# Optimization experiments

Measured on AMD Instinct MI355X. Metric: run time of the kernel, lower is better.

Reference implementation:

```python
import jax, jax.numpy as jnp
import numpy as np

# Straight-through binarization: forward hard threshold, backward identity.
# Matches BinarizeTensorThresh / BinarizedLinearFunction / BinaryActivation STE
# semantics from the diffnaps my_layers module (grad_weight = g^T x, i.e. the
# continuous weight receives the gradient of the binary weight unchanged).

def make_ste(thresh):
    @jax.custom_vjp
    def f(x):
        return (x >= thresh).astype(x.dtype)
    def fwd(x):
        return f(x), None
    def bwd(_, g):
        return (g,)
    f.defvjp(fwd, bwd)
    return f

ste_half = make_ste(0.5)  # weight binarization threshold (the 0.5 ctor arg)
ste_one = make_ste(1.0)   # activation fires when (pre-act + bias) >= 1

B, D, H, L = 4096, 5000, 2000, 50  # batch, input_dim(items), hidden_dim(patterns), label_dim
DATA_SPARSITY = 0.05


def setup_inputs() -> dict:
    key = jax.random.key(0)
    k = jax.random.split(key, 5)
    # sparse binary transaction data
    x = (jax.random.uniform(k[0], (B, D)) < DATA_SPARSITY).astype(jnp.float32)
    # continuous encoder weight in [0,1); binarized at 0.5 inside forward
    W_enc = jax.random.uniform(k[1], (H, D), dtype=jnp.float32)
    # small negative encoder bias (BinaPs-style init)
    b_enc = -jnp.abs(jax.random.normal(k[2], (H,), dtype=jnp.float32)) * 0.1
    act0_bias = jnp.zeros((H,), jnp.float32)
    act3_bias = jnp.zeros((D,), jnp.float32)
    # classifier_weight = logit(clip(N(0.1, 0.1), 0.01, 0.99)) as in __init__
    y = jnp.clip(0.1 + 0.1 * jax.random.normal(k[3], (L, H), dtype=jnp.float32), 0.01, 0.99)
    classifier_weight = jnp.log(y / (1.0 - y))
    return {
        "x": x,
        "W_enc": W_enc,
        "b_enc": b_enc,
        "act0_bias": act0_bias,
        "act3_bias": act3_bias,
        "classifier_weight": classifier_weight,
    }


def reference(x, W_enc, b_enc, act0_bias, act3_bias, classifier_weight):
    # fc0_enc: binarized-weight linear with bias
    Wb = ste_half(W_enc)                       # [H, D] in {0,1}
    h = x @ Wb.T + b_enc                       # [B, H]
    # act0: binary activation (threshold 1 on biased pre-activation)
    z = ste_one(h + act0_bias)                 # [B, H]
    # classify: sigmoid-gated classifier head (external_classifier=None / mode 'None')
    final_w = jax.nn.sigmoid(classifier_weight / 0.5)  # [L, H]
    classification = z @ final_w.T             # [B, L]
    # fc3_dec: shares the binarized encoder weight, transposed, no bias
    xd = z @ Wb                                # [B, D]
    output = ste_one(xd + act3_bias)           # [B, D]
    return output, classification, z
```

## Files before the change

### kernel.cpp

```cpp
#include <hip/hip_runtime.h>
#include <stdint.h>

static constexpr int Bn = 4096;
static constexpr int Dn = 5000;
static constexpr int Hn = 2000;
static constexpr int Ln = 50;
static constexpr int XW = 80;
static constexpr int Hpad = 2048;
static constexpr int Dpad = 5120;

typedef int v4i __attribute__((ext_vector_type(4)));
typedef int v16i __attribute__((ext_vector_type(16)));

#if defined(__has_builtin)
#if __has_builtin(__builtin_amdgcn_global_load_lds)
#define HAVE_GLOAD_LDS 1
#endif
#endif

#ifdef HAVE_GLOAD_LDS
__device__ __forceinline__ void gload16(const uint8_t* g, uint8_t* l) {
  __builtin_amdgcn_global_load_lds(
      (const __attribute__((address_space(1))) uint32_t*)g,
      (__attribute__((address_space(3))) uint32_t*)l, 16, 0, 0);
}
#endif

__device__ __forceinline__ int popc_acc(uint64_t v, int acc) {
  acc = __builtin_popcount((uint32_t)v) + acc;
  acc = __builtin_popcount((uint32_t)(v >> 32)) + acc;
  return acc;
}

__global__ void k_pack_xT(const float* __restrict__ x, uint8_t* __restrict__ xiT) {
  int g = (int)blockIdx.x * 256 + (int)threadIdx.x;
  int kb = g >> 12;
  int row = g & 4095;
  if (kb >= Dpad / 16) return;
  uint8_t o[16];
  int c0 = kb * 16;
  if (c0 + 15 < Dn) {
#pragma unroll
    for (int q = 0; q < 4; ++q) {
      float4 v = *(const float4*)(x + (size_t)row * Dn + c0 + q * 4);
      o[q * 4 + 0] = v.x >= 0.5f;
      o[q * 4 + 1] = v.y >= 0.5f;
      o[q * 4 + 2] = v.z >= 0.5f;
      o[q * 4 + 3] = v.w >= 0.5f;
    }
  } else {
#pragma unroll
    for (int e = 0; e < 16; ++e) {
      int c = c0 + e;
      o[e] = (c < Dn) ? (x[(size_t)row * Dn + c] >= 0.5f ? 1 : 0) : 0;
    }
  }
  *(uint4*)(xiT + ((size_t)kb * Bn + row) * 16) = *(uint4*)o;
}

__global__ __launch_bounds__(256) void k_pack_w_dualT(const float* __restrict__ W,
                                                      uint8_t* __restrict__ wi8T,
                                                      uint8_t* __restrict__ wtdT) {
  int d = (int)blockIdx.x * 256 + (int)threadIdx.x;
  int j0 = (int)blockIdx.y * 64;
  bool dv = d < Dn;
  int dc = d >> 4, de = d & 15;
  uint64_t colbits = 0;
  for (int r = 0; r < 64; ++r) {
    int j = j0 + r;
    float v = (j < Hn && dv) ? W[(size_t)j * Dn + d] : 0.0f;
    uint8_t bit = (v >= 0.5f) ? 1 : 0;
    wi8T[((size_t)dc * Hpad + j) * 16 + de] = bit;
    colbits |= ((uint64_t)bit) << r;
  }
#pragma unroll
  for (int q = 0; q < 4; ++q) {
    uint32_t u[4];
#pragma unroll
    for (int s = 0; s < 4; ++s) {
      uint32_t nib = (uint32_t)((colbits >> (q * 16 + s * 4)) & 0xFull);
      u[s] = (nib & 1u) | (((nib >> 1) & 1u) << 8) | (((nib >> 2) & 1u) << 16) |
             (((nib >> 3) & 1u) << 24);
    }
    *(uint4*)(wtdT + (((size_t)(j0 >> 4) + q) * Dpad + d) * 16) =
        make_uint4(u[0], u[1], u[2], u[3]);
  }
}

__global__ void k_pack_x(const float* __restrict__ x, uint64_t* __restrict__ xb2) {
  int g = (int)((blockIdx.x * blockDim.x + threadIdx.x) >> 6);
  int lane = (int)(threadIdx.x & 63);
  constexpr int nq = XW >> 2;
  int row = g / nq;
  int q = g - row * nq;
  if (row >= Bn) return;
  int w0 = q << 2;
  unsigned long long m[4];
#pragma unroll
  for (int e = 0; e < 4; ++e) {
    int col = ((w0 + e) << 6) + lane;
    float v = (col < Dn) ? x[(size_t)row * Dn + col] : 0.0f;
    m[e] = __ballot(v >= 0.5f);
  }
  if (lane < 4) {
    unsigned long long mv = m[0];
    mv = (lane == 1) ? m[1] : mv;
    mv = (lane == 2) ? m[2] : mv;
    mv = (lane == 3) ? m[3] : mv;
    int w = w0 + lane;
    xb2[((size_t)(w >> 1) * Bn + row) * 2 + (w & 1)] = mv;
  }
}

__global__ void k_pack_w(const float* __restrict__ W, uint64_t* __restrict__ wbT) {
  int g = (int)((blockIdx.x * blockDim.x + threadIdx.x) >> 6);
  int lane = (int)(threadIdx.x & 63);
  constexpr int nq = XW >> 2;
  int row = g / nq;
  int q = g - row * nq;
  if (row >= Hn) return;
  int w0 = q << 2;
  unsigned long long m[4];
#pragma unroll
  for (int e = 0; e < 4; ++e) {
    int col = ((w0 + e) << 6) + lane;
    float v = (col < Dn) ? W[(size_t)row * Dn + col] : 0.0f;
    m[e] = __ballot(v >= 0.5f);
  }
  if (lane < 4) {
    unsigned long long mv = m[0];
    mv = (lane == 1) ? m[1] : mv;
    mv = (lane == 2) ? m[2] : mv;
    mv = (lane == 3) ? m[3] : mv;
    wbT[(size_t)(w0 + lane) * Hpad + row] = mv;
  }
}

__global__ void k_transp(const uint64_t* __restrict__ wbT, uint32_t* __restrict__ wt32) {
  int g = (int)((blockIdx.x * blockDim.x + threadIdx.x) >> 6);
  int lane = (int)(threadIdx.x & 63);
  int w = g % XW;
  int jc = g / XW;
  if (jc >= Hpad / 64) return;
  uint64_t word = wbT[(size_t)w * Hpad + jc * 64 + lane];
  uint64_t mym = 0;
#pragma unroll
  for (int e = 0; e < 64; ++e) {
    unsigned long long m = __ballot((word >> e) & 1ull);
    mym = (lane == e) ? m : mym;
  }
  int d = w * 64 + lane;
  wt32[(size_t)(jc * 2) * Dpad + d] = (uint32_t)mym;
  wt32[(size_t)(jc * 2 + 1) * Dpad + d] = (uint32_t)(mym >> 32);
}

__global__ void k_pack_fwT(const float* __restrict__ cw, float* __restrict__ fwT) {
  int idx = blockIdx.x * blockDim.x + threadIdx.x;
  if (idx >= Hn * 64) return;
  int j = idx >> 6, l = idx & 63;
  float v = 0.0f;
  if (l < Ln) {
    float t = 2.0f * cw[(size_t)l * Hn + j];
    v = 1.0f / (1.0f + expf(-t));
  }
  fwT[idx] = v;
}

__global__ void k_zero(float* __restrict__ p, int n) {
  int i = blockIdx.x * blockDim.x + threadIdx.x;
  if (i < n) p[i] = 0.0f;
}


#ifdef HAVE_GLOAD_LDS
#define GEMM_PIPE(AROWS, BROWS, NT, Abase, Bbase)                               \
  const uint8_t* aS = (Abase) + ((size_t)bm * 128 + lane) * 16;                \
  const uint8_t* bS = (Bbase) + ((size_t)bn * 128 + lane) * 16;                \
  int kqw = 2 * wv;                           \
  _Pragma("unroll") for (int i = 0; i < 2; ++i) {                              \
    _Pragma("unroll") for (int c = 0; c < 2; ++c) {                            \
      gload16(aS + ((size_t)(kqw + i) * (AROWS) + c * 64) * 16,                \
              As + (kqw + i) * 2048 + c * 1024);                               \
      gload16(bS + ((size_t)(kqw + i) * (BROWS) + c * 64) * 16,                \
              Bs + (kqw + i) * 2048 + c * 1024);                               \
    }                                                                          \
  }                                                                            \
  __syncthreads();                                                             \
  int arow = wm * 64 + (lane & 31);                                            \
  int brow = wn * 64 + (lane & 31);                                            \
  int khalf = lane >> 5;                                                       \
  _Pragma("unroll 1") for (int t = 0; t < (NT); ++t) {                         \
    int cur = t & 1;                                                           \
    if (t + 1 < (NT)) {                                                        \
      size_t kb8 = (size_t)(t + 1) * 8;                                        \
      _Pragma("unroll") for (int i = 0; i < 2; ++i) {                          \
        _Pragma("unroll") for (int c = 0; c < 2; ++c) {                        \
          gload16(aS + ((kb8 + kqw + i) * (AROWS) + c * 64) * 16,              \
                  As + (cur ^ 1) * 16384 + (kqw + i) * 2048 + c * 1024);       \
          gload16(bS + ((kb8 + kqw + i) * (BROWS) + c * 64) * 16,              \
                  Bs + (cur ^ 1) * 16384 + (kqw + i) * 2048 + c * 1024);       \
        }                                                                      \
      }                                                                        \
    }                                                                          \
    const uint8_t* Ab = As + cur * 16384 + khalf * 2048;                       \
    const uint8_t* Bb = Bs + cur * 16384 + khalf * 2048;                       \
    _Pragma("unroll") for (int kk = 0; kk < 4; ++kk) {                         \
      v4i a0 = *(const v4i*)(Ab + kk * 4096 + arow * 16);                      \
      v4i a1 = *(const v4i*)(Ab + kk * 4096 + (arow + 32) * 16);               \
      v4i b0 = *(const v4i*)(Bb + kk * 4096 + brow * 16);                      \
      v4i b1 = *(const v4i*)(Bb + kk * 4096 + (brow + 32) * 16);               \
      acc[0][0] = __builtin_amdgcn_mfma_i32_32x32x32_i8(a0, b0, acc[0][0], 0, 0, 0); \
      acc[0][1] = __builtin_amdgcn_mfma_i32_32x32x32_i8(a0, b1, acc[0][1], 0, 0, 0); \
      acc[1][0] = __builtin_amdgcn_mfma_i32_32x32x32_i8(a1, b0, acc[1][0], 0, 0, 0); \
      acc[1][1] = __builtin_amdgcn_mfma_i32_32x32x32_i8(a1, b1, acc[1][1], 0, 0, 0); \
    }                                                                          \
    __syncthreads();                                                           \
  }
#else
#define GEMM_PIPE(AROWS, BROWS, NT, Abase, Bbase)                              \
  int skq = tid >> 5;                                                          \
  int sr4 = (tid & 31) * 4;                                                    \
  int arow = wm * 64 + (lane & 31);                                            \
  int brow = wn * 64 + (lane & 31);                                            \
  int khalf = lane >> 5;                                                       \
  _Pragma("unroll 1") for (int t = 0; t < (NT); ++t) {                         \
    size_t kb = (size_t)t * 8 + skq;                                           \
    v4i ra[4], rb[4];                                                          \
    _Pragma("unroll") for (int i = 0; i < 4; ++i) {                            \
      ra[i] = *(const v4i*)((Abase) + (kb * (AROWS) + bm * 128 + sr4 + i) * 16); \
      rb[i] = *(const v4i*)((Bbase) + (kb * (BROWS) + bn * 128 + sr4 + i) * 16); \
    }                                                                          \
    __syncthreads();                                                           \
    _Pragma("unroll") for (int i = 0; i < 4; ++i) {                            \
      *(v4i*)(As + skq * 2048 + (sr4 + i) * 16) = ra[i];                       \
      *(v4i*)(Bs + skq * 2048 + (sr4 + i) * 16) = rb[i];                       \
    }                                                                          \
    __syncthreads();                                                           \
    _Pragma("unroll") for (int kk = 0; kk < 4; ++kk) {                         \
      const uint8_t* Ab = As + (kk * 2 + khalf) * 2048;                        \
      const uint8_t* Bb = Bs + (kk * 2 + khalf) * 2048;                        \
      v4i a0 = *(const v4i*)(Ab + arow * 16);                                  \
      v4i a1 = *(const v4i*)(Ab + (arow + 32) * 16);                           \
      v4i b0 = *(const v4i*)(Bb + brow * 16);                                  \
      v4i b1 = *(const v4i*)(Bb + (brow + 32) * 16);                           \
      acc[0][0] = __builtin_amdgcn_mfma_i32_32x32x32_i8(a0, b0, acc[0][0], 0, 0, 0); \
      acc[0][1] = __builtin_amdgcn_mfma_i32_32x32x32_i8(a0, b1, acc[0][1], 0, 0, 0); \
      acc[1][0] = __builtin_amdgcn_mfma_i32_32x32x32_i8(a1, b0, acc[1][0], 0, 0, 0); \
      acc[1][1] = __builtin_amdgcn_mfma_i32_32x32x32_i8(a1, b1, acc[1][1], 0, 0, 0); \
    }                                                                          \
    __syncthreads();                                                           \
  }
#endif

__global__ __launch_bounds__(256) void k_enc_mfma(
    const uint8_t* __restrict__ A, const uint8_t* __restrict__ B,
    const float* __restrict__ b_enc, const float* __restrict__ act0b,
    float* __restrict__ z_out, uint8_t* __restrict__ zi8T) {
#ifdef HAVE_GLOAD_LDS
  __shared__ uint8_t As[2 * 16384];
  __shared__ uint8_t Bs[2 * 16384];
#else
  __shared__ uint8_t As[16384];
  __shared__ uint8_t Bs[16384];
#endif
  int tid = (int)threadIdx.x;
  int bn = (int)blockIdx.x;
  int bm = (int)blockIdx.y;
  int wv = __builtin_amdgcn_readfirstlane(tid >> 6);
  int lane = tid & 63;
  int wm = wv >> 1, wn = wv & 1;

  v16i acc[2][2];
#pragma unroll
  for (int i = 0; i < 2; ++i)
#pragma unroll
    for (int j = 0; j < 2; ++j) acc[i][j] = (v16i)0;

  GEMM_PIPE(Bn, Hpad, Dpad / 128, A, B)

  int col0 = bn * 128 + wn * 64 + (lane & 31);
#pragma unroll
  for (int ni = 0; ni < 2; ++ni) {
    int j = col0 + ni * 32;
    int js = (j < Hn) ? j : (Hn - 1);
    float be = b_enc[js];
    float ab = act0b[js];
    bool jv = j < Hn;
#pragma unroll
    for (int mi = 0; mi < 2; ++mi) {
      int rbase = bm * 128 + wm * 64 + mi * 32;
#pragma unroll
      for (int r = 0; r < 16; ++r) {
        int rloc = (r & 3) + 8 * (r >> 2) + 4 * (lane >> 5);
        int b = rbase + rloc;
        float h = ((float)acc[mi][ni][r] + be) + ab;
        bool zb = jv && (h >= 1.0f);
        if (jv) {
          z_out[(size_t)b * Hn + j] = zb ? 1.0f : 0.0f;
          zi8T[((size_t)(j >> 4) * Bn + b) * 16 + (j & 15)] = zb ? 1 : 0;
        }
      }
    }
  }
}

__global__ __launch_bounds__(256) void k_dec_mfma(
    const uint8_t* __restrict__ A,
    const uint8_t* __restrict__ B,
    const float* __restrict__ act3b, float* __restrict__ out) {
#ifdef HAVE_GLOAD_LDS
  __shared__ uint8_t As[2 * 16384];
  __shared__ uint8_t Bs[2 * 16384];
#else
  __shared__ uint8_t As[16384];
  __shared__ uint8_t Bs[16384];
#endif
  int tid = (int)threadIdx.x;
  int bn = (int)blockIdx.x;
  int bm = (int)blockIdx.y;
  int wv = __builtin_amdgcn_readfirstlane(tid >> 6);
  int lane = tid & 63;
  int wm = wv >> 1, wn = wv & 1;

  v16i acc[2][2];
#pragma unroll
  for (int i = 0; i < 2; ++i)
#pragma unroll
    for (int j = 0; j < 2; ++j) acc[i][j] = (v16i)0;

  GEMM_PIPE(Bn, Dpad, Hpad / 128, A, B)

  int col0 = bn * 128 + wn * 64 + (lane & 31);
#pragma unroll
  for (int ni = 0; ni < 2; ++ni) {
    int d = col0 + ni * 32;
    int ds = (d < Dn) ? d : (Dn - 1);
    float ab = act3b[ds];
    bool dv = d < Dn;
#pragma unroll
    for (int mi = 0; mi < 2; ++mi) {
      int rbase = bm * 128 + wm * 64 + mi * 32;
#pragma unroll
      for (int r = 0; r < 16; ++r) {
        int rloc = (r & 3) + 8 * (r >> 2) + 4 * (lane >> 5);
        int b = rbase + rloc;
        if (dv) out[(size_t)b * Dn + d] = (((float)acc[mi][ni][r] + ab) >= 1.0f) ? 1.0f : 0.0f;
      }
    }
  }
}

__global__ __launch_bounds__(256) void k_enc_bit(const uint64_t* __restrict__ xb2,
                                                 const uint64_t* __restrict__ wbT,
                                                 const float* __restrict__ b_enc,
                                                 const float* __restrict__ act0b,
                                                 float* __restrict__ z_out,
                                                 uint8_t* __restrict__ zb8) {
  __shared__ uint64_t wl[XW][8];
  int tid = (int)threadIdx.x;
  int jg = (int)blockIdx.x;
  int j0 = jg << 3;
#pragma unroll
  for (int k = 0; k < 3; ++k) {
    int idx = k * 256 + tid;
    if (idx < XW * 8) {
      int w = idx >> 3, j = idx & 7;
      wl[w][j] = wbT[(size_t)w * Hpad + j0 + j];
    }
  }
  __syncthreads();
  int wv = __builtin_amdgcn_readfirstlane(tid >> 6);
  int lane = tid & 63;
  int bg = (int)blockIdx.y * 4 + wv;
  int b0 = (bg << 8) + lane;
  int acc[4][8] = {};
  const uint64_t* xp = xb2 + 2 * (size_t)b0;
#pragma unroll 1
  for (int w2 = 0; w2 < XW / 2; ++w2) {
    ulong2 xx[4];
#pragma unroll
    for (int i = 0; i < 4; ++i)
      xx[i] = *(const ulong2*)(xp + ((size_t)w2 * Bn + i * 64) * 2);
#pragma unroll
    for (int t2 = 0; t2 < 4; ++t2) {
      ulong2 wa = *(ulong2*)&wl[2 * w2][2 * t2];
      ulong2 wb = *(ulong2*)&wl[2 * w2 + 1][2 * t2];
#pragma unroll
      for (int i = 0; i < 4; ++i) {
        acc[i][2 * t2]     = popc_acc(xx[i].x & wa.x, acc[i][2 * t2]);
        acc[i][2 * t2 + 1] = popc_acc(xx[i].x & wa.y, acc[i][2 * t2 + 1]);
        acc[i][2 * t2]     = popc_acc(xx[i].y & wb.x, acc[i][2 * t2]);
        acc[i][2 * t2 + 1] = popc_acc(xx[i].y & wb.y, acc[i][2 * t2 + 1]);
      }
    }
  }
  float be[8], ab[8];
#pragma unroll
  for (int t = 0; t < 8; ++t) {
    int j = j0 + t;
    int js = (j < Hn) ? j : (Hn - 1);
    be[t] = b_enc[js];
    ab[t] = act0b[js];
  }
#pragma unroll
  for (int i = 0; i < 4; ++i) {
    int b = b0 + i * 64;
    uint32_t zbyte = 0;
    float zf[8];
#pragma unroll
    for (int t = 0; t < 8; ++t) {
      int j = j0 + t;
      float h = ((float)acc[i][t] + be[t]) + ab[t];
      bool zb = (j < Hn) && (h >= 1.0f);
      zbyte |= zb ? (1u << t) : 0u;
      zf[t] = zb ? 1.0f : 0.0f;
    }
    zb8[((size_t)(jg >> 2) * Bn + b) * 4 + (jg & 3)] = (uint8_t)zbyte;
    if (j0 < Hn) {
      float* zp = z_out + (size_t)b * Hn + j0;
      *(float4*)zp = make_float4(zf[0], zf[1], zf[2], zf[3]);
      *(float4*)(zp + 4) = make_float4(zf[4], zf[5], zf[6], zf[7]);
    }
  }
}

__global__ __launch_bounds__(256, 6) void k_dec_bit(const uint32_t* __restrict__ zb32,
                                                    const uint32_t* __restrict__ wt32,
                                                    const float* __restrict__ act3b,
                                                    float* __restrict__ out) {
  __shared__ uint32_t tl[64][8];
  int tid = (int)threadIdx.x;
  int dc = (int)blockIdx.x;
  int d0 = dc << 3;
  {
#pragma unroll
    for (int k = 0; k < 2; ++k) {
      int e = k * 256 + tid;
      int hw = e >> 3, dl = e & 7;
      tl[hw][dl] = wt32[(size_t)hw * Dpad + d0 + dl];
    }
  }
  __syncthreads();
  int wv = __builtin_amdgcn_readfirstlane(tid >> 6);
  int lane = tid & 63;
  int bg = (int)blockIdx.y * 4 + wv;
  int b0 = (bg << 8) + lane;
  int acc[4][8] = {};
  const uint32_t* zp = zb32 + b0;
  uint32_t z0, z1, z2, z3, n0, n1, n2, n3;
  uint4 wA, wB, wAn, wBn;
  z0 = zp[0]; z1 = zp[64]; z2 = zp[128]; z3 = zp[192];
  wA = *(const uint4*)&tl[0][0];
  wB = *(const uint4*)&tl[0][4];
#define DEC_MAC()                                          \
  do {                                                     \
    acc[0][0] = __builtin_popcount(z0 & wA.x) + acc[0][0]; \
    acc[0][1] = __builtin_popcount(z0 & wA.y) + acc[0][1]; \
    acc[0][2] = __builtin_popcount(z0 & wA.z) + acc[0][2]; \
    acc[0][3] = __builtin_popcount(z0 & wA.w) + acc[0][3]; \
    acc[0][4] = __builtin_popcount(z0 & wB.x) + acc[0][4]; \
    acc[0][5] = __builtin_popcount(z0 & wB.y) + acc[0][5]; \
    acc[0][6] = __builtin_popcount(z0 & wB.z) + acc[0][6]; \
    acc[0][7] = __builtin_popcount(z0 & wB.w) + acc[0][7]; \
    acc[1][0] = __builtin_popcount(z1 & wA.x) + acc[1][0]; \
    acc[1][1] = __builtin_popcount(z1 & wA.y) + acc[1][1]; \
    acc[1][2] = __builtin_popcount(z1 & wA.z) + acc[1][2]; \
    acc[1][3] = __builtin_popcount(z1 & wA.w) + acc[1][3]; \
    acc[1][4] = __builtin_popcount(z1 & wB.x) + acc[1][4]; \
    acc[1][5] = __builtin_popcount(z1 & wB.y) + acc[1][5]; \
    acc[1][6] = __builtin_popcount(z1 & wB.z) + acc[1][6]; \
    acc[1][7] = __builtin_popcount(z1 & wB.w) + acc[1][7]; \
    acc[2][0] = __builtin_popcount(z2 & wA.x) + acc[2][0]; \
    acc[2][1] = __builtin_popcount(z2 & wA.y) + acc[2][1]; \
    acc[2][2] = __builtin_popcount(z2 & wA.z) + acc[2][2]; \
    acc[2][3] = __builtin_popcount(z2 & wA.w) + acc[2][3]; \
    acc[2][4] = __builtin_popcount(z2 & wB.x) + acc[2][4]; \
    acc[2][5] = __builtin_popcount(z2 & wB.y) + acc[2][5]; \
    acc[2][6] = __builtin_popcount(z2 & wB.z) + acc[2][6]; \
    acc[2][7] = __builtin_popcount(z2 & wB.w) + acc[2][7]; \
    acc[3][0] = __builtin_popcount(z3 & wA.x) + acc[3][0]; \
    acc[3][1] = __builtin_popcount(z3 & wA.y) + acc[3][1]; \
    acc[3][2] = __builtin_popcount(z3 & wA.z) + acc[3][2]; \
    acc[3][3] = __builtin_popcount(z3 & wA.w) + acc[3][3]; \
    acc[3][4] = __builtin_popcount(z3 & wB.x) + acc[3][4]; \
    acc[3][5] = __builtin_popcount(z3 & wB.y) + acc[3][5]; \
    acc[3][6] = __builtin_popcount(z3 & wB.z) + acc[3][6]; \
    acc[3][7] = __builtin_popcount(z3 & wB.w) + acc[3][7]; \
  } while (0)
#pragma unroll 1
  for (int hw = 0; hw < 64; ++hw) {
    int hn = (hw < 63) ? hw + 1 : hw;
    const uint32_t* zq = zp + (size_t)hn * Bn;
    n0 = zq[0]; n1 = zq[64]; n2 = zq[128]; n3 = zq[192];
    wAn = *(const uint4*)&tl[hn][0];
    wBn = *(const uint4*)&tl[hn][4];
    DEC_MAC();
    z0 = n0; z1 = n1; z2 = n2; z3 = n3;
    wA = wAn; wB = wBn;
  }
#undef DEC_MAC
  float ab[8];
#pragma unroll
  for (int t = 0; t < 8; ++t) {
    int d = d0 + t;
    int ds = (d < Dn) ? d : (Dn - 1);
    ab[t] = act3b[ds];
  }
  if (d0 < Dn) {
#pragma unroll
    for (int i = 0; i < 4; ++i) {
      int b = b0 + i * 64;
      float of[8];
#pragma unroll
      for (int t = 0; t < 8; ++t)
        of[t] = (((float)acc[i][t] + ab[t]) >= 1.0f) ? 1.0f : 0.0f;
      float* op = out + (size_t)b * Dn + d0;
      *(float4*)op = make_float4(of[0], of[1], of[2], of[3]);
      *(float4*)(op + 4) = make_float4(of[4], of[5], of[6], of[7]);
    }
  }
}

__global__ __launch_bounds__(256) void k_cls_i8(const uint8_t* __restrict__ zi8T,
                                                const float* __restrict__ fwT,
                                                float* __restrict__ cls) {
  __shared__ float zT[64][132];
  __shared__ float fwL[64][64];
  int tid = (int)threadIdx.x;
  int bb0 = (int)blockIdx.x * 128;
  int jsp = (int)blockIdx.y;
  int tx = tid & 15, ty = tid >> 4;
  float acc[8][4] = {};
  for (int tile = 0; tile < 4; ++tile) {
    int jt0 = jsp * 256 + tile * 64;
    __syncthreads();
#pragma unroll
    for (int k = 0; k < 8; ++k) {
      int idx = k * 256 + tid;
      int r = idx >> 4, c4 = idx & 15;
      int j = jt0 + c4 * 4;
      uchar4 v = make_uchar4(0, 0, 0, 0);
      if (j < Hn)
        v = *(const uchar4*)(zi8T + ((size_t)(j >> 4) * Bn + (bb0 + r)) * 16 + (j & 15));
      zT[c4 * 4 + 0][r] = (float)v.x;
      zT[c4 * 4 + 1][r] = (float)v.y;
      zT[c4 * 4 + 2][r] = (float)v.z;
      zT[c4 * 4 + 3][r] = (float)v.w;
    }
#pragma unroll
    for (int k = 0; k < 4; ++k) {
      int idx = k * 256 + tid;
      int jj = idx >> 4, c4 = idx & 15;
      int j = jt0 + jj;
      float4 v = make_float4(0.f, 0.f, 0.f, 0.f);
      if (j < Hn) v = *(const float4*)(fwT + (size_t)j * 64 + c4 * 4);
      *(float4*)&fwL[jj][c4 * 4] = v;
    }
    __syncthreads();
#pragma unroll 4
    for (int jj = 0; jj < 64; ++jj) {
      float4 fv = *(float4*)&fwL[jj][tx * 4];
      float4 za = *(float4*)&zT[jj][ty * 8];
      float4 zb = *(float4*)&zT[jj][ty * 8 + 4];
      float zz[8] = {za.x, za.y, za.z, za.w, zb.x, zb.y, zb.z, zb.w};
      float ff[4] = {fv.x, fv.y, fv.z, fv.w};
#pragma unroll
      for (int i = 0; i < 8; ++i)
#pragma unroll
        for (int l = 0; l < 4; ++l) acc[i][l] += zz[i] * ff[l];
    }
  }
#pragma unroll
  for (int i = 0; i < 8; ++i) {
    int b = bb0 + ty * 8 + i;
#pragma unroll
    for (int l = 0; l < 4; ++l) {
      int L = tx * 4 + l;
      if (L < Ln) atomicAdd(&cls[(size_t)b * Ln + L], acc[i][l]);
    }
  }
}

__global__ __launch_bounds__(256) void k_cls_f32(const float* __restrict__ z,
                                                 const float* __restrict__ fwT,
                                                 float* __restrict__ cls) {
  __shared__ float zT[64][132];
  __shared__ float fwL[64][64];
  int tid = (int)threadIdx.x;
  int bb0 = (int)blockIdx.x * 128;
  int jsp = (int)blockIdx.y;
  int tx = tid & 15, ty = tid >> 4;
  float acc[8][4] = {};
  for (int tile = 0; tile < 4; ++tile) {
    int jt0 = jsp * 256 + tile * 64;
    __syncthreads();
#pragma unroll
    for (int k = 0; k < 8; ++k) {
      int idx = k * 256 + tid;
      int r = idx >> 4, c4 = idx & 15;
      int j = jt0 + c4 * 4;
      float4 v = make_float4(0.f, 0.f, 0.f, 0.f);
      if (j < Hn) v = *(const float4*)(z + (size_t)(bb0 + r) * Hn + j);
      zT[c4 * 4 + 0][r] = v.x;
      zT[c4 * 4 + 1][r] = v.y;
      zT[c4 * 4 + 2][r] = v.z;
      zT[c4 * 4 + 3][r] = v.w;
    }
#pragma unroll
    for (int k = 0; k < 4; ++k) {
      int idx = k * 256 + tid;
      int jj = idx >> 4, c4 = idx & 15;
      int j = jt0 + jj;
      float4 v = make_float4(0.f, 0.f, 0.f, 0.f);
      if (j < Hn) v = *(const float4*)(fwT + (size_t)j * 64 + c4 * 4);
      *(float4*)&fwL[jj][c4 * 4] = v;
    }
    __syncthreads();
#pragma unroll 4
    for (int jj = 0; jj < 64; ++jj) {
      float4 fv = *(float4*)&fwL[jj][tx * 4];
      float4 za = *(float4*)&zT[jj][ty * 8];
      float4 zb = *(float4*)&zT[jj][ty * 8 + 4];
      float zz[8] = {za.x, za.y, za.z, za.w, zb.x, zb.y, zb.z, zb.w};
      float ff[4] = {fv.x, fv.y, fv.z, fv.w};
#pragma unroll
      for (int i = 0; i < 8; ++i)
#pragma unroll
        for (int l = 0; l < 4; ++l) acc[i][l] += zz[i] * ff[l];
    }
  }
#pragma unroll
  for (int i = 0; i < 8; ++i) {
    int b = bb0 + ty * 8 + i;
#pragma unroll
    for (int l = 0; l < 4; ++l) {
      int L = tx * 4 + l;
      if (L < Ln) atomicAdd(&cls[(size_t)b * Ln + L], acc[i][l]);
    }
  }
}

extern "C" void kernel_launch(void* const* d_in, const int* in_sizes, int n_in,
                              void* d_out, int out_size, void* d_ws, size_t ws_size,
                              hipStream_t stream) {
  const float* x     = (const float*)d_in[0];
  const float* W     = (const float*)d_in[1];
  const float* b_enc = (const float*)d_in[2];
  const float* act0b = (const float*)d_in[3];
  const float* act3b = (const float*)d_in[4];
  const float* cw    = (const float*)d_in[5];

  float* out0 = (float*)d_out;
  float* cls  = out0 + (size_t)Bn * Dn;
  float* zout = cls + (size_t)Bn * Ln;

  char* p = (char*)d_ws;
  uint32_t* zb32 = (uint32_t*)p; p += (size_t)64 * Bn * 4;
  float*    fwT  = (float*)p;    p += (size_t)Hn * 64 * 4;
  size_t common = (size_t)(p - (char*)d_ws);

  size_t sz_xi8 = (size_t)Bn * Dpad;
  size_t sz_wi8 = (size_t)Hpad * Dpad;
  size_t sz_zi8 = (size_t)Bn * Hpad;
  size_t sz_wtd = (size_t)Dpad * Hpad;
  size_t sz_wbT = (size_t)XW * Hpad * 8;
  size_t sz_wt32 = (size_t)64 * Dpad * 4;
  size_t full_need = common + sz_xi8 + sz_wi8 + sz_zi8 + sz_wtd;

  k_pack_fwT<<<(Hn * 64 + 255) / 256, 256, 0, stream>>>(cw, fwT);
  k_zero<<<(Bn * Ln + 255) / 256, 256, 0, stream>>>(cls, Bn * Ln);

  if (ws_size >= full_need) {
    uint8_t* xiT  = (uint8_t*)p;
    uint8_t* wi8T = xiT + sz_xi8;
    uint8_t* zi8T = wi8T + sz_wi8;
    uint8_t* wtdT = zi8T + sz_zi8;
    k_pack_xT<<<(Dpad / 16) * Bn / 256, 256, 0, stream>>>(x, xiT);
    dim3 gwd(Dpad / 256, Hpad / 64);
    k_pack_w_dualT<<<gwd, 256, 0, stream>>>(W, wi8T, wtdT);
    dim3 ge(Hpad / 128, Bn / 128);
    k_enc_mfma<<<ge, 256, 0, stream>>>(xiT, wi8T, b_enc, act0b, zout, zi8T);
    dim3 g3(32, 8);
    k_cls_i8<<<g3, 256, 0, stream>>>(zi8T, fwT, cls);
    dim3 gd(Dpad / 128, Bn / 128);
    k_dec_mfma<<<gd, 256, 0, stream>>>(zi8T, wtdT, act3b, out0);
  } else {
    uint64_t* wbT  = (uint64_t*)p;
    uint32_t* wt32 = (uint32_t*)(p + sz_wbT);
    uint64_t* xb2  = (uint64_t*)(p + sz_wbT + sz_wt32);
    {
      long long waves = (long long)Hn * (XW / 4);
      k_pack_w<<<(int)((waves * 64 + 255) / 256), 256, 0, stream>>>(W, wbT);
    }
    {
      long long waves = (long long)(Hpad / 64) * XW;
      k_transp<<<(int)((waves * 64 + 255) / 256), 256, 0, stream>>>(wbT, wt32);
    }
    {
      long long waves = (long long)Bn * (XW / 4);
      k_pack_x<<<(int)((waves * 64 + 255) / 256), 256, 0, stream>>>(x, xb2);
    }
    dim3 g1(256, 4);
    k_enc_bit<<<g1, 256, 0, stream>>>(xb2, wbT, b_enc, act0b, zout, (uint8_t*)zb32);
    dim3 g3(32, 8);
    k_cls_f32<<<g3, 256, 0, stream>>>(zout, fwT, cls);
    dim3 g2(640, 4);
    k_dec_bit<<<g2, 256, 0, stream>>>(zb32, wt32, act3b, out0);
  }
}
```

Before: 238.4 us.

## Load A operand directly into registers, stage only B through LDS

The A tile is no longer staged in shared memory. Each wave loads its own A fragments from global memory straight into registers, double-buffered in two register sets, while B keeps the LDS double buffer. The main loop is unrolled by two to alternate between the register and LDS buffers. This cuts LDS footprint and LDS traffic, which may allow higher occupancy. In exchange it raises VGPR pressure, duplicates global loads of A across the two wn waves, and assumes NT is even (the loop steps by 2 and stages t+1 unconditionally).

```diff
diff --git a/kernel.cpp b/kernel.cpp
--- a/kernel.cpp
+++ b/kernel.cpp
@@ -173,47 +173,57 @@
 
 
 #ifdef HAVE_GLOAD_LDS
-#define GEMM_PIPE(AROWS, BROWS, NT, Abase, Bbase)                               \
-  const uint8_t* aS = (Abase) + ((size_t)bm * 128 + lane) * 16;                \
-  const uint8_t* bS = (Bbase) + ((size_t)bn * 128 + lane) * 16;                \
-  int kqw = 2 * wv;                           \
-  _Pragma("unroll") for (int i = 0; i < 2; ++i) {                              \
-    _Pragma("unroll") for (int c = 0; c < 2; ++c) {                            \
-      gload16(aS + ((size_t)(kqw + i) * (AROWS) + c * 64) * 16,                \
-              As + (kqw + i) * 2048 + c * 1024);                               \
-      gload16(bS + ((size_t)(kqw + i) * (BROWS) + c * 64) * 16,                \
-              Bs + (kqw + i) * 2048 + c * 1024);                               \
-    }                                                                          \
-  }                                                                            \
-  __syncthreads();                                                             \
+#define GP_DECL(AROWS, BROWS, Abase, Bbase)                                    \
+  const uint8_t* bS = (Bbase) + ((size_t)bn * 128 + lane) * 16;               \
+  int kqw = 2 * wv;                                                            \
   int arow = wm * 64 + (lane & 31);                                            \
   int brow = wn * 64 + (lane & 31);                                            \
   int khalf = lane >> 5;                                                       \
-  _Pragma("unroll 1") for (int t = 0; t < (NT); ++t) {                         \
-    int cur = t & 1;                                                           \
-    if (t + 1 < (NT)) {                                                        \
-      size_t kb8 = (size_t)(t + 1) * 8;                                        \
-      _Pragma("unroll") for (int i = 0; i < 2; ++i) {                          \
-        _Pragma("unroll") for (int c = 0; c < 2; ++c) {                        \
-          gload16(aS + ((kb8 + kqw + i) * (AROWS) + c * 64) * 16,              \
-                  As + (cur ^ 1) * 16384 + (kqw + i) * 2048 + c * 1024);       \
-          gload16(bS + ((kb8 + kqw + i) * (BROWS) + c * 64) * 16,              \
-                  Bs + (cur ^ 1) * 16384 + (kqw + i) * 2048 + c * 1024);       \
-        }                                                                      \
-      }                                                                        \
+  const uint8_t* aR0 = (Abase) + ((size_t)(bm * 128 + arow)) * 16;             \
+  const uint8_t* aR1 = aR0 + 32 * 16;                                          \
+  v4i aA[2][4], aB[2][4];
+
+#define GP_STAGE_B(AROWSX, BROWS, buf, tt)                                     \
+  _Pragma("unroll") for (int i = 0; i < 2; ++i) {                              \
+    _Pragma("unroll") for (int c = 0; c < 2; ++c) {                            \
+      gload16(bS + (((size_t)(tt) * 8 + kqw + i) * (BROWS) + c * 64) * 16,     \
+              Bs + (buf) * 16384 + (kqw + i) * 2048 + c * 1024);               \
     }                                                                          \
-    const uint8_t* Ab = As + cur * 16384 + khalf * 2048;                       \
-    const uint8_t* Bb = Bs + cur * 16384 + khalf * 2048;                       \
-    _Pragma("unroll") for (int kk = 0; kk < 4; ++kk) {                         \
-      v4i a0 = *(const v4i*)(Ab + kk * 4096 + arow * 16);                      \
-      v4i a1 = *(const v4i*)(Ab + kk * 4096 + (arow + 32) * 16);               \
-      v4i b0 = *(const v4i*)(Bb + kk * 4096 + brow * 16);                      \
-      v4i b1 = *(const v4i*)(Bb + kk * 4096 + (brow + 32) * 16);               \
-      acc[0][0] = __builtin_amdgcn_mfma_i32_32x32x32_i8(a0, b0, acc[0][0], 0, 0, 0); \
-      acc[0][1] = __builtin_amdgcn_mfma_i32_32x32x32_i8(a0, b1, acc[0][1], 0, 0, 0); \
-      acc[1][0] = __builtin_amdgcn_mfma_i32_32x32x32_i8(a1, b0, acc[1][0], 0, 0, 0); \
-      acc[1][1] = __builtin_amdgcn_mfma_i32_32x32x32_i8(a1, b1, acc[1][1], 0, 0, 0); \
+  }
+
+#define GP_LOAD_A(AROWS, dst, tt)                                              \
+  _Pragma("unroll") for (int kk = 0; kk < 4; ++kk) {                           \
+    size_t pl = ((size_t)(tt) * 8 + kk * 2 + khalf) * (size_t)(AROWS) * 16;    \
+    dst[0][kk] = *(const v4i*)(aR0 + pl);                                      \
+    dst[1][kk] = *(const v4i*)(aR1 + pl);                                      \
+  }
+
+#define GP_COMPUTE(aset, buf)                                                  \
+  _Pragma("unroll") for (int kk = 0; kk < 4; ++kk) {                           \
+    const uint8_t* Bb = Bs + (buf) * 16384 + (kk * 2 + khalf) * 2048;          \
+    v4i b0 = *(const v4i*)(Bb + brow * 16);                                    \
+    v4i b1 = *(const v4i*)(Bb + (brow + 32) * 16);                             \
+    acc[0][0] = __builtin_amdgcn_mfma_i32_32x32x32_i8(aset[0][kk], b0, acc[0][0], 0, 0, 0); \
+    acc[0][1] = __builtin_amdgcn_mfma_i32_32x32x32_i8(aset[0][kk], b1, acc[0][1], 0, 0, 0); \
+    acc[1][0] = __builtin_amdgcn_mfma_i32_32x32x32_i8(aset[1][kk], b0, acc[1][0], 0, 0, 0); \
+    acc[1][1] = __builtin_amdgcn_mfma_i32_32x32x32_i8(aset[1][kk], b1, acc[1][1], 0, 0, 0); \
+  }
+
+#define GEMM_PIPE(AROWS, BROWS, NT, Abase, Bbase)                              \
+  GP_DECL(AROWS, BROWS, Abase, Bbase)                                          \
+  GP_STAGE_B(AROWS, BROWS, 0, 0)                                               \
+  GP_LOAD_A(AROWS, aA, 0)                                                      \
+  __syncthreads();                                                             \
+  _Pragma("unroll 1") for (int t = 0; t < (NT); t += 2) {                      \
+    GP_STAGE_B(AROWS, BROWS, 1, t + 1)                                         \
+    GP_LOAD_A(AROWS, aB, t + 1)                                                \
+    GP_COMPUTE(aA, 0)                                                          \
+    __syncthreads();                                                           \
+    if (t + 2 < (NT)) {                                                        \
+      GP_STAGE_B(AROWS, BROWS, 0, t + 2)                                       \
+      GP_LOAD_A(AROWS, aA, t + 2)                                              \
     }                                                                          \
+    GP_COMPUTE(aB, 1)                                                          \
     __syncthreads();                                                           \
   }
 #else
@@ -257,7 +267,6 @@
     const float* __restrict__ b_enc, const float* __restrict__ act0b,
     float* __restrict__ z_out, uint8_t* __restrict__ zi8T) {
 #ifdef HAVE_GLOAD_LDS
-  __shared__ uint8_t As[2 * 16384];
   __shared__ uint8_t Bs[2 * 16384];
 #else
   __shared__ uint8_t As[16384];
@@ -309,7 +318,6 @@
     const uint8_t* __restrict__ B,
     const float* __restrict__ act3b, float* __restrict__ out) {
 #ifdef HAVE_GLOAD_LDS
-  __shared__ uint8_t As[2 * 16384];
   __shared__ uint8_t Bs[2 * 16384];
 #else
   __shared__ uint8_t As[16384];
```

After: 236.1 us. About the same (-0.9%).

## Deepen GEMM LDS prefetch to two stages with explicit vmcnt waits

Applied to the files above, without the earlier changes.

Restructures the global-to-LDS pipeline so two k-tiles are in flight. The loop now waits with partial vmcnt counts and raw s_barrier instead of draining everything at each __syncthreads, and issues the load for tile t+2 into the buffer just consumed. It also raises wave priority around the MFMA block with s_setprio. This should hide more global load latency behind compute, at the cost of two barriers per iteration and hand-tuned waitcnt values that must match the number of outstanding loads.

```diff
diff --git a/kernel.cpp b/kernel.cpp
--- a/kernel.cpp
+++ b/kernel.cpp
@@ -176,34 +176,31 @@
 #define GEMM_PIPE(AROWS, BROWS, NT, Abase, Bbase)                               \
   const uint8_t* aS = (Abase) + ((size_t)bm * 128 + lane) * 16;                \
   const uint8_t* bS = (Bbase) + ((size_t)bn * 128 + lane) * 16;                \
-  int kqw = 2 * wv;                           \
-  _Pragma("unroll") for (int i = 0; i < 2; ++i) {                              \
-    _Pragma("unroll") for (int c = 0; c < 2; ++c) {                            \
-      gload16(aS + ((size_t)(kqw + i) * (AROWS) + c * 64) * 16,                \
-              As + (kqw + i) * 2048 + c * 1024);                               \
-      gload16(bS + ((size_t)(kqw + i) * (BROWS) + c * 64) * 16,                \
-              Bs + (kqw + i) * 2048 + c * 1024);                               \
-    }                                                                          \
-  }                                                                            \
-  __syncthreads();                                                             \
+  int kqw = 2 * wv;                                                            \
   int arow = wm * 64 + (lane & 31);                                            \
   int brow = wn * 64 + (lane & 31);                                            \
   int khalf = lane >> 5;                                                       \
+  auto STAGE = [&](int buf, int tt) {                                          \
+    _Pragma("unroll") for (int i = 0; i < 2; ++i) {                            \
+      _Pragma("unroll") for (int c = 0; c < 2; ++c) {                          \
+        gload16(aS + (((size_t)tt * 8 + kqw + i) * (AROWS) + c * 64) * 16,     \
+                As + buf * 16384 + (kqw + i) * 2048 + c * 1024);               \
+        gload16(bS + (((size_t)tt * 8 + kqw + i) * (BROWS) + c * 64) * 16,     \
+                Bs + buf * 16384 + (kqw + i) * 2048 + c * 1024);               \
+      }                                                                        \
+    }                                                                          \
+  };                                                                           \
+  STAGE(0, 0);                                                                 \
+  STAGE(1, 1);                                                                 \
+  asm volatile("s_waitcnt vmcnt(8)" ::: "memory");                             \
+  __builtin_amdgcn_sched_barrier(0);                                           \
+  __builtin_amdgcn_s_barrier();                                                \
+  __builtin_amdgcn_sched_barrier(0);                                           \
   _Pragma("unroll 1") for (int t = 0; t < (NT); ++t) {                         \
     int cur = t & 1;                                                           \
-    if (t + 1 < (NT)) {                                                        \
-      size_t kb8 = (size_t)(t + 1) * 8;                                        \
-      _Pragma("unroll") for (int i = 0; i < 2; ++i) {                          \
-        _Pragma("unroll") for (int c = 0; c < 2; ++c) {                        \
-          gload16(aS + ((kb8 + kqw + i) * (AROWS) + c * 64) * 16,              \
-                  As + (cur ^ 1) * 16384 + (kqw + i) * 2048 + c * 1024);       \
-          gload16(bS + ((kb8 + kqw + i) * (BROWS) + c * 64) * 16,              \
-                  Bs + (cur ^ 1) * 16384 + (kqw + i) * 2048 + c * 1024);       \
-        }                                                                      \
-      }                                                                        \
-    }                                                                          \
     const uint8_t* Ab = As + cur * 16384 + khalf * 2048;                       \
     const uint8_t* Bb = Bs + cur * 16384 + khalf * 2048;                       \
+    __builtin_amdgcn_s_setprio(1);                                             \
     _Pragma("unroll") for (int kk = 0; kk < 4; ++kk) {                         \
       v4i a0 = *(const v4i*)(Ab + kk * 4096 + arow * 16);                      \
       v4i a1 = *(const v4i*)(Ab + kk * 4096 + (arow + 32) * 16);               \
@@ -214,7 +211,19 @@
       acc[1][0] = __builtin_amdgcn_mfma_i32_32x32x32_i8(a1, b0, acc[1][0], 0, 0, 0); \
       acc[1][1] = __builtin_amdgcn_mfma_i32_32x32x32_i8(a1, b1, acc[1][1], 0, 0, 0); \
     }                                                                          \
-    __syncthreads();                                                           \
+    __builtin_amdgcn_s_setprio(0);                                             \
+    __builtin_amdgcn_sched_barrier(0);                                         \
+    __builtin_amdgcn_s_barrier();         \
+    __builtin_amdgcn_sched_barrier(0);                                         \
+    if (t + 2 < (NT)) {                                                        \
+      STAGE(cur, t + 2);                                                       \
+      asm volatile("s_waitcnt vmcnt(8)" ::: "memory");         \
+    } else {                                                                   \
+      asm volatile("s_waitcnt vmcnt(0)" ::: "memory");         \
+    }                                                                          \
+    __builtin_amdgcn_sched_barrier(0);                                         \
+    __builtin_amdgcn_s_barrier();             \
+    __builtin_amdgcn_sched_barrier(0);                                         \
   }
 #else
 #define GEMM_PIPE(AROWS, BROWS, NT, Abase, Bbase)                              \
```

Result: no change. 242.5 us (+1.7%).
